# Kernel tuning notes

Hardware: AMD Instinct MI355X
Metric: run time of the kernel (lower is better)

## Reference

```python
import jax, jax.numpy as jnp
import numpy as np

B, I, P, T = 128, 64, 16, 5
N_TYPE, VOCAB, D = 3, 100000, 64


def setup_inputs() -> dict:
    key = jax.random.key(0)
    k1, k2, k3, k4, k5 = jax.random.split(key, 5)
    path_input = jax.random.randint(k1, (B, I, P, T), 0, VOCAB, dtype=jnp.int32)
    path_type = jax.random.randint(k2, (T,), 0, N_TYPE, dtype=jnp.int32)
    tables = jax.random.normal(k3, (N_TYPE, VOCAB, D), dtype=jnp.float32) * 0.02
    # nn.Conv1d(D, D, 2): weight [out=D, in=D, k=2], bias [D]
    bound = 1.0 / np.sqrt(D * 2)
    conv_w = jax.random.uniform(k4, (D, D, 2), minval=-bound, maxval=bound, dtype=jnp.float32)
    conv_b = jax.random.uniform(k5, (D,), minval=-bound, maxval=bound, dtype=jnp.float32)
    return {"path_input": path_input, "path_type": path_type,
            "tables": tables, "conv_w": conv_w, "conv_b": conv_b}


def reference(path_input, path_type, tables, conv_w, conv_b):
    b, i, p, t = path_input.shape
    n = b * i
    d = tables.shape[-1]
    vocab = tables.shape[1]
    x = path_input.reshape(n, p, t)
    # per-timestep dynamic-table gather, fused via flat indexing:
    # element (n,p,j) looks up row x[n,p,j] of table path_type[j]
    flat_idx = path_type[None, None, :].astype(jnp.int32) * vocab + x  # [n,p,t]
    emb = tables.reshape(-1, d)[flat_idx]                              # [n,p,t,d]
    # Conv1d kernel_size=2 over the time axis (valid): windows of 2
    xw = jnp.stack([emb[:, :, :-1, :], emb[:, :, 1:, :]], axis=-1)     # [n,p,t-1,d,2]
    y = jnp.einsum('nptik,oik->npto', xw, conv_w) + conv_b             # [n,p,t-1,d]
    # max-pool over remaining time positions (NOTE: no ReLU in original forward)
    pooled = jnp.max(y, axis=2)                                        # [n,p,d]
    # faithful replication of torch.cat(outputs,-1).view(p, n, d) memory trick
    out = pooled.reshape(n, p * d).reshape(p, n, d)                    # [p,n,d]
    out = jnp.max(jnp.transpose(out, (1, 2, 0)), axis=-1)              # [n,d]
    return out.reshape(b, i, d)
```

## Files before the change

### kernel.cpp

```cpp
#include <hip/hip_runtime.h>
#include <hip/hip_bf16.h>

#define B_  128
#define I_  64
#define P_  16
#define T_  5
#define NT  3
#define VOCAB 100000
#define D_  64
#define NPAIR (B_ * I_)
#define OUTROWS NPAIR

__device__ __forceinline__ unsigned short f2b(float f) {
    unsigned int u = __float_as_uint(f);
    return (unsigned short)((u + 0x7fffu + ((u >> 16) & 1u)) >> 16);
}

typedef short short8 __attribute__((ext_vector_type(8)));
typedef float f32x4 __attribute__((ext_vector_type(4)));

__global__ __launch_bounds__(256) void wprep(
        const float* __restrict__ convw, unsigned short* __restrict__ Wf) {
    const int e0 = threadIdx.x * 4;
#pragma unroll
    for (int e = e0; e < e0 + 4; ++e) {
        int m = e & 15;
        int quad = (e >> 4) & 3;
        int half = (e >> 6) & 1;
        int cb = e >> 7;
        int c = cb * 16 + m;
        const float* wp = (c < 64) ? (convw + c * 128) : (convw + (c - 64) * 128 + 1);
#pragma unroll
        for (int j = 0; j < 8; ++j) {
            int k = half * 32 + quad * 8 + j;
            Wf[e * 8 + j] = f2b(wp[k * 2]);
        }
    }
}

__global__ __launch_bounds__(256) void fused_path(
        const int* __restrict__ path_input, const int* __restrict__ path_type,
        const float* __restrict__ tables, const unsigned short* __restrict__ Wf,
        const float* __restrict__ bias, float* __restrict__ out) {
    const int tid = threadIdx.x;
    const int w = tid >> 6;
    const int lane = tid & 63;
    const int l16 = lane & 15;
    const int quad = lane >> 4;

    const int nn = blockIdx.x * 4 + w;
    const int g = nn >> 4, q = nn & 15;

    short8 WB0[8], WB1[8];
#pragma unroll
    for (int ns = 0; ns < 8; ++ns) {
        WB0[ns] = *(const short8*)&Wf[((ns * 8 + 0 + quad) * 16 + l16) * 8];
        WB1[ns] = *(const short8*)&Wf[((ns * 8 + 4 + quad) * 16 + l16) * 8];
    }

    int rows[5];
#pragma unroll
    for (int t = 0; t < 5; ++t) {
        int addr = ((l16 * 512 + g) * 16 + q) * 5 + t;
        rows[t] = path_type[t] * VOCAB + path_input[addr];
    }

    float4 F[20];
#pragma unroll
    for (int t = 0; t < 5; ++t) {
        const float* rp = tables + (size_t)rows[t] * 64;
        F[t * 4 + 0] = *(const float4*)(rp + quad * 8);
        F[t * 4 + 1] = *(const float4*)(rp + quad * 8 + 4);
        F[t * 4 + 2] = *(const float4*)(rp + 32 + quad * 8);
        F[t * 4 + 3] = *(const float4*)(rp + 32 + quad * 8 + 4);
    }

    short8 A0[5], A1[5];
#pragma unroll
    for (int t = 0; t < 5; ++t) {
        float4 fa = F[t * 4 + 0], fb = F[t * 4 + 1];
        float4 fc = F[t * 4 + 2], fd = F[t * 4 + 3];
        short8 a0, a1;
        a0[0] = (short)f2b(fa.x); a0[1] = (short)f2b(fa.y);
        a0[2] = (short)f2b(fa.z); a0[3] = (short)f2b(fa.w);
        a0[4] = (short)f2b(fb.x); a0[5] = (short)f2b(fb.y);
        a0[6] = (short)f2b(fb.z); a0[7] = (short)f2b(fb.w);
        a1[0] = (short)f2b(fc.x); a1[1] = (short)f2b(fc.y);
        a1[2] = (short)f2b(fc.z); a1[3] = (short)f2b(fc.w);
        a1[4] = (short)f2b(fd.x); a1[5] = (short)f2b(fd.y);
        a1[6] = (short)f2b(fd.z); a1[7] = (short)f2b(fd.w);
        A0[t] = a0; A1[t] = a1;
    }

    f32x4 runmax[4];
#pragma unroll
    for (int ns = 0; ns < 4; ++ns) runmax[ns] = (f32x4){-1e30f, -1e30f, -1e30f, -1e30f};
#pragma unroll
    for (int to = 0; to < 4; ++to) {
#pragma unroll
        for (int ns = 0; ns < 4; ++ns) {
            f32x4 uu = {0.f, 0.f, 0.f, 0.f};
            uu = __builtin_amdgcn_mfma_f32_16x16x32_bf16(WB0[ns], A0[to], uu, 0, 0, 0);
            uu = __builtin_amdgcn_mfma_f32_16x16x32_bf16(WB1[ns], A1[to], uu, 0, 0, 0);
            f32x4 vv = {0.f, 0.f, 0.f, 0.f};
            vv = __builtin_amdgcn_mfma_f32_16x16x32_bf16(WB0[ns + 4], A0[to + 1], vv, 0, 0, 0);
            vv = __builtin_amdgcn_mfma_f32_16x16x32_bf16(WB1[ns + 4], A1[to + 1], vv, 0, 0, 0);
#pragma unroll
            for (int j = 0; j < 4; ++j)
                runmax[ns][j] = fmaxf(runmax[ns][j], uu[j] + vv[j]);
        }
    }

#pragma unroll
    for (int ns = 0; ns < 4; ++ns) {
#pragma unroll
        for (int j = 0; j < 4; ++j) {
            float v = runmax[ns][j];
            v = fmaxf(v, __shfl_xor(v, 1));
            v = fmaxf(v, __shfl_xor(v, 2));
            v = fmaxf(v, __shfl_xor(v, 4));
            v = fmaxf(v, __shfl_xor(v, 8));
            runmax[ns][j] = v;
        }
    }
    if (l16 == 0) {
#pragma unroll
        for (int ns = 0; ns < 4; ++ns) {
            int c = ns * 16 + quad * 4;
            float4 bv = *(const float4*)(bias + c);
            float4 o;
            o.x = runmax[ns][0] + bv.x;
            o.y = runmax[ns][1] + bv.y;
            o.z = runmax[ns][2] + bv.z;
            o.w = runmax[ns][3] + bv.w;
            *(float4*)(out + (size_t)nn * 64 + c) = o;
        }
    }
}

__global__ __launch_bounds__(64) void fused_direct(
        const int* __restrict__ path_input, const int* __restrict__ path_type,
        const float* __restrict__ tables, const float* __restrict__ convw,
        const float* __restrict__ bias, float* __restrict__ out) {
    const int nn = blockIdx.x;
    const int o = threadIdx.x;
    const int g = nn >> 4;
    const int q = nn & 15;
    float w0[64], w1[64];
#pragma unroll
    for (int i = 0; i < 64; ++i) {
        w0[i] = convw[o * 128 + i * 2];
        w1[i] = convw[o * 128 + i * 2 + 1];
    }
    int tb[5];
#pragma unroll
    for (int t = 0; t < 5; ++t) tb[t] = path_type[t] * VOCAB;
    __shared__ float emb[5][64];
    float acc = -1e30f;
    for (int pp = 0; pp < 16; ++pp) {
        int m = pp * 512 + g;
        const int* ip = path_input + ((m * 16 + q) * 5);
        __syncthreads();
#pragma unroll
        for (int t = 0; t < 5; ++t)
            emb[t][o] = tables[(size_t)(tb[t] + ip[t]) * 64 + o];
        __syncthreads();
#pragma unroll
        for (int to = 0; to < 4; ++to) {
            float s = 0.f;
#pragma unroll
            for (int i = 0; i < 64; ++i)
                s += w0[i] * emb[to][i] + w1[i] * emb[to + 1][i];
            acc = fmaxf(acc, s);
        }
    }
    out[(size_t)nn * 64 + o] = acc + bias[o];
}

extern "C" void kernel_launch(void* const* d_in, const int* in_sizes, int n_in,
                              void* d_out, int out_size, void* d_ws, size_t ws_size,
                              hipStream_t stream) {
    const int*   path_input = (const int*)d_in[0];
    const int*   path_type  = (const int*)d_in[1];
    const float* tables     = (const float*)d_in[2];
    const float* convw      = (const float*)d_in[3];
    const float* convb      = (const float*)d_in[4];
    float* out = (float*)d_out;

    const size_t needWf = (size_t)16 * 1024 * sizeof(unsigned short);
    if (ws_size >= needWf) {
        unsigned short* Wf = (unsigned short*)d_ws;
        wprep<<<1, 256, 0, stream>>>(convw, Wf);
        fused_path<<<OUTROWS / 4, 256, 0, stream>>>(path_input, path_type,
                                                    tables, Wf, convb, out);
    } else {
        fused_direct<<<OUTROWS, 64, 0, stream>>>(path_input, path_type, tables, convw, convb, out);
    }
}
```

Before: 144.5 us.

## Coalesce embedding row gathers via LDS staging before MFMA fragment loads

Each embedding row is now fetched by 16 lanes reading consecutive float4s, so one row is one contiguous 256-byte access, instead of each lane reading four scattered 32-byte pieces. The rows are converted to bf16 and written to a per-wave shared-memory tile with padded stride, then read back in MFMA A-fragment layout. This is meant to cut gather transaction count and improve memory coalescing on the random table lookups. In exchange it adds a shared-memory round trip, about 51KB of LDS per block that may limit occupancy, and more index loads per lane.

```diff
diff --git a/kernel.cpp b/kernel.cpp
--- a/kernel.cpp
+++ b/kernel.cpp
@@ -19,6 +19,9 @@
 typedef short short8 __attribute__((ext_vector_type(8)));
 typedef float f32x4 __attribute__((ext_vector_type(4)));
 
+#define AROW_STRIDE 160
+#define AWAVE_BYTES (80 * AROW_STRIDE)
+
 __global__ __launch_bounds__(256) void wprep(
         const float* __restrict__ convw, unsigned short* __restrict__ Wf) {
     const int e0 = threadIdx.x * 4;
@@ -42,14 +45,18 @@
         const int* __restrict__ path_input, const int* __restrict__ path_type,
         const float* __restrict__ tables, const unsigned short* __restrict__ Wf,
         const float* __restrict__ bias, float* __restrict__ out) {
+    __shared__ __align__(16) unsigned char Asmem[4][AWAVE_BYTES];
     const int tid = threadIdx.x;
     const int w = tid >> 6;
     const int lane = tid & 63;
     const int l16 = lane & 15;
     const int quad = lane >> 4;
+    const int r2 = lane >> 4;
+    const int c16 = lane & 15;
 
     const int nn = blockIdx.x * 4 + w;
     const int g = nn >> 4, q = nn & 15;
+    unsigned char* myA = Asmem[w];
 
     short8 WB0[8], WB1[8];
 #pragma unroll
@@ -58,38 +65,36 @@
         WB1[ns] = *(const short8*)&Wf[((ns * 8 + 4 + quad) * 16 + l16) * 8];
     }
 
-    int rows[5];
+    int roff[20];
+#pragma unroll
+    for (int i = 0; i < 20; ++i) {
+        int t = i >> 2, sub = i & 3;
+        int pp = sub * 4 + r2;
+        int addr = ((pp * 512 + g) * 16 + q) * 5 + t;
+        roff[i] = (path_type[t] * VOCAB + path_input[addr]) * 64;
+    }
+
+    float4 F[20];
+#pragma unroll
+    for (int i = 0; i < 20; ++i)
+        F[i] = *(const float4*)(tables + (size_t)roff[i] + c16 * 4);
+
+#pragma unroll
+    for (int i = 0; i < 20; ++i) {
+        int t = i >> 2, sub = i & 3;
+        int R = t * 16 + sub * 4 + r2;
+        unsigned int p0 = (unsigned int)f2b(F[i].x) | ((unsigned int)f2b(F[i].y) << 16);
+        unsigned int p1 = (unsigned int)f2b(F[i].z) | ((unsigned int)f2b(F[i].w) << 16);
+        uint2 pk; pk.x = p0; pk.y = p1;
+        *(uint2*)(myA + R * AROW_STRIDE + c16 * 8) = pk;
+    }
+
+    short8 A0[5], A1[5];
 #pragma unroll
     for (int t = 0; t < 5; ++t) {
-        int addr = ((l16 * 512 + g) * 16 + q) * 5 + t;
-        rows[t] = path_type[t] * VOCAB + path_input[addr];
-    }
-
-    float4 F[20];
-#pragma unroll
-    for (int t = 0; t < 5; ++t) {
-        const float* rp = tables + (size_t)rows[t] * 64;
-        F[t * 4 + 0] = *(const float4*)(rp + quad * 8);
-        F[t * 4 + 1] = *(const float4*)(rp + quad * 8 + 4);
-        F[t * 4 + 2] = *(const float4*)(rp + 32 + quad * 8);
-        F[t * 4 + 3] = *(const float4*)(rp + 32 + quad * 8 + 4);
-    }
-
-    short8 A0[5], A1[5];
-#pragma unroll
-    for (int t = 0; t < 5; ++t) {
-        float4 fa = F[t * 4 + 0], fb = F[t * 4 + 1];
-        float4 fc = F[t * 4 + 2], fd = F[t * 4 + 3];
-        short8 a0, a1;
-        a0[0] = (short)f2b(fa.x); a0[1] = (short)f2b(fa.y);
-        a0[2] = (short)f2b(fa.z); a0[3] = (short)f2b(fa.w);
-        a0[4] = (short)f2b(fb.x); a0[5] = (short)f2b(fb.y);
-        a0[6] = (short)f2b(fb.z); a0[7] = (short)f2b(fb.w);
-        a1[0] = (short)f2b(fc.x); a1[1] = (short)f2b(fc.y);
-        a1[2] = (short)f2b(fc.z); a1[3] = (short)f2b(fc.w);
-        a1[4] = (short)f2b(fd.x); a1[5] = (short)f2b(fd.y);
-        a1[6] = (short)f2b(fd.z); a1[7] = (short)f2b(fd.w);
-        A0[t] = a0; A1[t] = a1;
+        const unsigned char* rp = myA + (t * 16 + l16) * AROW_STRIDE;
+        A0[t] = *(const short8*)(rp + quad * 16);
+        A1[t] = *(const short8*)(rp + 64 + quad * 16);
     }
 
     f32x4 runmax[4];
```

Result: faster. 132.8 us (-8.1%).
